# Kernel tuning notes

Measured on AMD Instinct MI355X. Metric: run time of the kernel, lower is better.

The kernel has to match this reference:

```python
import jax, jax.numpy as jnp
import numpy as np

LATENT_DIM = 64
K = 128


def setup_inputs() -> dict:
    key = jax.random.key(0)
    ks = jax.random.split(key, 7)
    B, T, N, d, k = 64, 1024, 1024, LATENT_DIM, K
    return {
        "review_seq": jax.random.normal(ks[0], (B, T, d), dtype=jnp.float32),
        "post_seq": jax.random.normal(ks[1], (B, N, d), dtype=jnp.float32),
        "Wl": jax.random.normal(ks[2], (d, d), dtype=jnp.float32) * 0.05,
        "Wr": jax.random.normal(ks[3], (k, d), dtype=jnp.float32) * 0.05,
        "Wp": jax.random.normal(ks[4], (k, d), dtype=jnp.float32) * 0.05,
        "whr": jax.random.normal(ks[5], (1, k), dtype=jnp.float32) * 0.05,
        "whp": jax.random.normal(ks[6], (1, k), dtype=jnp.float32) * 0.05,
    }


def reference(review_seq, post_seq, Wl, Wr, Wp, whr, whp):
    # L[b,t,n] = tanh(review @ Wl @ post^T)
    L = jnp.tanh(jnp.einsum('btd,dD,bnD->btn', review_seq, Wl, post_seq))
    # Hp[b,k,n] = tanh(Wp @ post^T + Wr @ review^T @ L)
    Hp = jnp.tanh(jnp.einsum('kd,bnd->bkn', Wp, post_seq)
                  + jnp.einsum('kd,btd,btn->bkn', Wr, review_seq, L))
    # Hr[b,k,t] = tanh(Wr @ review^T + Wp @ post^T @ L^T)
    Hr = jnp.tanh(jnp.einsum('kd,btd->bkt', Wr, review_seq)
                  + jnp.einsum('kd,bnd,btn->bkt', Wp, post_seq, L))
    # attention weights over post (n) and review (t) positions
    Ap = jax.nn.softmax(jnp.einsum('yk,bkn->bn', whp, Hp), axis=-1)
    Ar = jax.nn.softmax(jnp.einsum('yk,bkt->bt', whr, Hr), axis=-1)
    co_p = jnp.einsum('bnd,bn->bd', post_seq, Ap)
    co_r = jnp.einsum('btd,bt->bd', review_seq, Ar)
    return jnp.concatenate([co_p, co_r], axis=1)  # [B, 2*latent_dim]
```

## Files before the change

kernel.cpp:

```cpp
#include <hip/hip_runtime.h>
#include <hip/hip_bf16.h>


typedef __attribute__((ext_vector_type(8))) short bfrag;
typedef __attribute__((ext_vector_type(4))) float ffrag;

typedef const __attribute__((address_space(1))) unsigned GAS_U;
typedef __attribute__((address_space(3))) unsigned LAS_U;

__device__ __forceinline__ void gload16(const void* g, void* l) {
  __builtin_amdgcn_global_load_lds((GAS_U*)g, (LAS_U*)l, 16, 0, 0);
}

__device__ __forceinline__ unsigned short f2b(float f) {
  unsigned u = __builtin_bit_cast(unsigned, f);
  u += 0x7FFFu + ((u >> 16) & 1u);
  return (unsigned short)(u >> 16);
}
__device__ __forceinline__ float b2f(unsigned short h) {
  return __builtin_bit_cast(float, (unsigned)h << 16);
}
__device__ __forceinline__ float ftanh(float x) {
  float e = __builtin_amdgcn_exp2f(x * 2.88539008177792681f);
  return fmaf(-2.0f, __builtin_amdgcn_rcpf(e + 1.0f), 1.0f);
}
__device__ __forceinline__ unsigned cvtpk(float lo, float hi) {
  unsigned r;
  asm("v_cvt_pk_bf16_f32 %0, %1, %2" : "=v"(r) : "v"(lo), "v"(hi));
  return r;
}

#define MFMA(a, b, c) __builtin_amdgcn_mfma_f32_16x16x32_bf16((a), (b), (c), 0, 0, 0)


__global__ __launch_bounds__(256) void prep_kernel(
    const float* __restrict__ review, const float* __restrict__ post,
    const float* __restrict__ Wl, const float* __restrict__ Wr,
    const float* __restrict__ Wp,
    unsigned short* __restrict__ RWb, unsigned short* __restrict__ Rb,
    unsigned short* __restrict__ Pb, unsigned short* __restrict__ postb)
{
  const int chunk = blockIdx.x, b = blockIdx.y, side = blockIdx.z;
  const int tid = threadIdx.x, lane = tid & 63, w = tid >> 6;
  const int lr = lane & 15, lg = lane >> 4;
  const int r0 = chunk * 128;

  __shared__ __align__(16) unsigned short seqs[128][72];
  __shared__ __align__(16) unsigned short wgt[128][72];
  __shared__ __align__(16) unsigned short wlt[64][72];

  const float* seq = (side == 0) ? review : post;
#pragma unroll
  for (int jj = 0; jj < 8; ++jj) {
    int e = tid + jj * 256;
    int r = e >> 4, d4 = (e & 15) * 4;
    float4 v = *(const float4*)(seq + ((size_t)(b * 1024 + r0 + r)) * 64 + d4);
    unsigned lo = ((unsigned)f2b(v.y) << 16) | f2b(v.x);
    unsigned hi = ((unsigned)f2b(v.w) << 16) | f2b(v.z);
    *(uint2*)&seqs[r][d4] = make_uint2(lo, hi);
    if (side == 1)
      *(uint2*)(postb + ((size_t)(b * 1024 + r0 + r)) * 64 + d4) = make_uint2(lo, hi);
  }
  const float* wkd = (side == 0) ? Wr : Wp;
#pragma unroll
  for (int jj = 0; jj < 8; ++jj) {
    int e = tid + jj * 256;
    int k = e >> 4, d4 = (e & 15) * 4;
    float4 v = *(const float4*)(wkd + k * 64 + d4);
    unsigned lo = ((unsigned)f2b(v.y) << 16) | f2b(v.x);
    unsigned hi = ((unsigned)f2b(v.w) << 16) | f2b(v.z);
    *(uint2*)&wgt[k][d4] = make_uint2(lo, hi);
  }
  if (side == 0) {
    for (int i = tid; i < 64 * 64; i += 256) {
      int d = i >> 6, c = i & 63;
      wlt[c][d] = f2b(Wl[d * 64 + c]);
    }
  }
  __syncthreads();

  if (side == 0) {
    ffrag acc[2][4] = {};
#pragma unroll
    for (int ks = 0; ks < 2; ++ks)
#pragma unroll
      for (int is = 0; is < 4; ++is) {
        bfrag a = *(const bfrag*)&wlt[is * 16 + lr][ks * 32 + lg * 8];
#pragma unroll
        for (int tt = 0; tt < 2; ++tt) {
          bfrag bb = *(const bfrag*)&seqs[(w * 2 + tt) * 16 + lr][ks * 32 + lg * 8];
          acc[tt][is] = MFMA(a, bb, acc[tt][is]);
        }
      }
#pragma unroll
    for (int tt = 0; tt < 2; ++tt) {
      const int t = r0 + (w * 2 + tt) * 16 + lr;
      char* rowb = (char*)RWb + ((size_t)(b * 1024 + t)) * 128 + lg * 8;
#pragma unroll
      for (int is = 0; is < 4; ++is) {
        uint2 pkv;
        pkv.x = cvtpk(acc[tt][is][0], acc[tt][is][1]);
        pkv.y = cvtpk(acc[tt][is][2], acc[tt][is][3]);
        *(uint2*)(rowb + is * 32) = pkv;
      }
    }
  }
  {
    ffrag acc[2][8] = {};
#pragma unroll
    for (int ks = 0; ks < 2; ++ks)
#pragma unroll
      for (int tt = 0; tt < 2; ++tt) {
        bfrag a = *(const bfrag*)&seqs[(w * 2 + tt) * 16 + lr][ks * 32 + lg * 8];
#pragma unroll
        for (int kt = 0; kt < 8; ++kt) {
          bfrag bb = *(const bfrag*)&wgt[kt * 16 + lr][ks * 32 + lg * 8];
          acc[tt][kt] = MFMA(a, bb, acc[tt][kt]);
        }
      }
    char* dstb = (char*)((side == 0) ? Rb : Pb) + (size_t)b * 262144
                 + (size_t)(chunk * 4 + w) * 8192 + lg * 256 + lr * 16;
#pragma unroll
    for (int tt = 0; tt < 2; ++tt)
#pragma unroll
      for (int kt = 0; kt < 8; ++kt) {
        uint2 pkv;
        pkv.x = cvtpk(acc[tt][kt][0], acc[tt][kt][1]);
        pkv.y = cvtpk(acc[tt][kt][2], acc[tt][kt][3]);
        *(uint2*)(dstb + kt * 1024 + tt * 8) = pkv;
      }
  }
}

__global__ __launch_bounds__(512, 4) void hz_kernel(
    const unsigned short* __restrict__ RWb, const unsigned short* __restrict__ Rb,
    const unsigned short* __restrict__ Pb, const unsigned short* __restrict__ postb,
    const float* __restrict__ whp, const float* __restrict__ whr,
    float* __restrict__ zp, float* __restrict__ zr)
{
  const int orig = blockIdx.x;
  const int swz = (orig & 7) * 128 + (orig >> 3);
  const int strip = swz & 7, pair = swz >> 3;
  const int b = pair & 63, role = pair >> 6;
  const int s0 = strip * 128;
  const int tid = threadIdx.x, lane = tid & 63, w = tid >> 6;
  const int lr = lane & 15, lg = lane >> 4;

  const unsigned short* resident = role ? RWb : postb;
  const unsigned short* chunkseq = role ? postb : RWb;
  const unsigned short* coeff    = role ? Pb : Rb;
  const unsigned short* addterm  = role ? Rb : Pb;
  const float* wh                = role ? whr : whp;
  float* zout                    = role ? zr : zp;

  __shared__ __align__(16) char smem[24576];
  const int woff = w << 10;

  const int crow = tid >> 3, cslot = tid & 7;
  const char* csrc = (const char*)chunkseq + (size_t)b * 131072
                     + crow * 128 + ((cslot ^ (crow & 7)) << 4);
  const char* ksrc = (const char*)coeff + (size_t)b * 262144 + tid * 16;

  bfrag rb[2];
  {
    const char* rbase = (const char*)resident + ((size_t)(b * 1024 + s0)) * 128
                        + (w * 16 + lr) * 128 + lg * 16;
    rb[0] = *(const bfrag*)(rbase);
    rb[1] = *(const bfrag*)(rbase + 64);
  }

  if (w < 4) gload16(csrc, smem + woff);
  gload16(ksrc, smem + 8192 + woff);
  __syncthreads();

  ffrag acc[8] = {};

#pragma unroll 1
  for (int tc = 0; tc < 32; ++tc) {
    const int cur = tc & 1, nb = cur ^ 1;
    if (tc < 31) {
      if (w < 4) gload16(csrc + (size_t)(tc + 1) * 4096, smem + nb * 4096 + woff);
      gload16(ksrc + (size_t)(tc + 1) * 8192, smem + 8192 + nb * 8192 + woff);
    }

    const char* rwc = smem + cur * 4096;
    uint2 pk[2];
#pragma unroll
    for (int ts = 0; ts < 2; ++ts) {
      ffrag la = {};
#pragma unroll
      for (int ks = 0; ks < 2; ++ks) {
        const int arow = ts * 16 + lr;
        bfrag a = *(const bfrag*)(rwc + arow * 128 + (((ks * 4 + lg) ^ (arow & 7)) << 4));
        la = MFMA(a, rb[ks], la);
      }
      pk[ts].x = cvtpk(ftanh(la[0]), ftanh(la[1]));
      pk[ts].y = cvtpk(ftanh(la[2]), ftanh(la[3]));
    }
    uint4 au; au.x = pk[0].x; au.y = pk[0].y; au.z = pk[1].x; au.w = pk[1].y;
    const bfrag af = __builtin_bit_cast(bfrag, au);

    const char* rlc = smem + 8192 + cur * 8192 + lg * 256 + lr * 16;
#pragma unroll
    for (int kt = 0; kt < 8; ++kt) {
      bfrag bk = *(const bfrag*)(rlc + kt * 1024);
      acc[kt] = MFMA(af, bk, acc[kt]);
    }
    __syncthreads();
  }

  float whs[8];
#pragma unroll
  for (int kt = 0; kt < 8; ++kt) whs[kt] = wh[kt * 16 + lr];

  const char* abase = (const char*)addterm + (size_t)b * 262144
                      + (size_t)(strip * 4 + (w >> 1)) * 8192
                      + lg * 256 + lr * 16 + (w & 1) * 8;
  float zs[4] = {0, 0, 0, 0};
#pragma unroll
  for (int kt = 0; kt < 8; ++kt) {
    uint2 av = *(const uint2*)(abase + kt * 1024);
    const float whk = whs[kt];
    zs[0] += whk * ftanh(acc[kt][0] + b2f((unsigned short)(av.x & 0xFFFF)));
    zs[1] += whk * ftanh(acc[kt][1] + b2f((unsigned short)(av.x >> 16)));
    zs[2] += whk * ftanh(acc[kt][2] + b2f((unsigned short)(av.y & 0xFFFF)));
    zs[3] += whk * ftanh(acc[kt][3] + b2f((unsigned short)(av.y >> 16)));
  }
#pragma unroll
  for (int j = 0; j < 4; ++j) {
    zs[j] += __shfl_xor(zs[j], 1);
    zs[j] += __shfl_xor(zs[j], 2);
    zs[j] += __shfl_xor(zs[j], 4);
    zs[j] += __shfl_xor(zs[j], 8);
  }
  if (lr == 0) {
#pragma unroll
    for (int j = 0; j < 4; ++j)
      zout[(size_t)b * 1024 + s0 + w * 16 + lg * 4 + j] = zs[j];
  }
}

__global__ __launch_bounds__(1024) void final_kernel(
    const float* __restrict__ review, const float* __restrict__ post,
    const float* __restrict__ zp, const float* __restrict__ zr,
    float* __restrict__ out)
{
  const int b = blockIdx.x, side = blockIdx.y, tid = threadIdx.x;
  const int wid = tid >> 6, lane = tid & 63;
  __shared__ float zl[1024];
  __shared__ float red[16];
  __shared__ float cacc[16][64];

  const float* z = (side == 0) ? zp : zr;
  const float* seq = (side == 0) ? post : review;

  float v = z[(size_t)b * 1024 + tid];
  zl[tid] = v;
  float m = v;
#pragma unroll
  for (int off = 32; off; off >>= 1) m = fmaxf(m, __shfl_xor(m, off));
  if (lane == 0) red[wid] = m;
  __syncthreads();
  m = red[0];
#pragma unroll
  for (int i = 1; i < 16; ++i) m = fmaxf(m, red[i]);
  __syncthreads();

  float e = __expf(v - m);
  zl[tid] = e;
  float sm = e;
#pragma unroll
  for (int off = 32; off; off >>= 1) sm += __shfl_xor(sm, off);
  if (lane == 0) red[wid] = sm;
  __syncthreads();
  sm = red[0];
#pragma unroll
  for (int i = 1; i < 16; ++i) sm += red[i];
  const float inv = 1.0f / sm;

  const int d = lane;
  float a = 0.f;
  for (int n = wid * 64; n < wid * 64 + 64; ++n)
    a += zl[n] * seq[((size_t)(b * 1024 + n)) * 64 + d];
  cacc[wid][d] = a;
  __syncthreads();
  if (tid < 64) {
    float s = 0.f;
#pragma unroll
    for (int g = 0; g < 16; ++g) s += cacc[g][tid];
    out[b * 128 + side * 64 + tid] = s * inv;
  }
}

extern "C" void kernel_launch(void* const* d_in, const int* in_sizes, int n_in,
                              void* d_out, int out_size, void* d_ws, size_t ws_size,
                              hipStream_t stream) {
  const float* review = (const float*)d_in[0];
  const float* post   = (const float*)d_in[1];
  const float* Wl     = (const float*)d_in[2];
  const float* Wr     = (const float*)d_in[3];
  const float* Wp     = (const float*)d_in[4];
  const float* whr    = (const float*)d_in[5];
  const float* whp    = (const float*)d_in[6];
  float* out = (float*)d_out;

  char* ws = (char*)d_ws;
  unsigned short* RWb   = (unsigned short*)(ws);
  unsigned short* Rb    = (unsigned short*)(ws + (size_t)8  * 1048576);
  unsigned short* Pb    = (unsigned short*)(ws + (size_t)24 * 1048576);
  unsigned short* postb = (unsigned short*)(ws + (size_t)40 * 1048576);
  float* zp = (float*)(ws + (size_t)48 * 1048576);
  float* zr = (float*)(ws + (size_t)48 * 1048576 + 262144);

  prep_kernel<<<dim3(8, 64, 2), dim3(256), 0, stream>>>(
      review, post, Wl, Wr, Wp, RWb, Rb, Pb, postb);
  hz_kernel<<<dim3(1024), dim3(512), 0, stream>>>(
      RWb, Rb, Pb, postb, whp, whr, zp, zr);
  final_kernel<<<dim3(64, 2), dim3(1024), 0, stream>>>(
      review, post, zp, zr, out);
}
```

Baseline: 99.29 us.

## Double per-block strip width so each chunk load feeds two row tiles

Each hz_kernel block now covers 256 resident rows instead of 128, with each wave holding two 16-row resident fragments and two accumulator sets. Every streamed chunk of the other sequence and the coefficient matrix staged in shared memory is reused for twice as many MFMAs, which halves the global/LDS traffic for the streamed operands and halves the grid to 512 blocks. The cost is more registers per thread (two acc[8] sets) and fewer blocks to fill the GPU, which may reduce occupancy or leave CUs idle.

```diff
diff --git a/kernel.cpp b/kernel.cpp
--- a/kernel.cpp
+++ b/kernel.cpp
@@ -139,10 +139,10 @@
     float* __restrict__ zp, float* __restrict__ zr)
 {
   const int orig = blockIdx.x;
-  const int swz = (orig & 7) * 128 + (orig >> 3);
-  const int strip = swz & 7, pair = swz >> 3;
+  const int swz = (orig & 7) * 64 + (orig >> 3);
+  const int strip = swz & 3, pair = swz >> 2;
   const int b = pair & 63, role = pair >> 6;
-  const int s0 = strip * 128;
+  const int s0 = strip * 256;
   const int tid = threadIdx.x, lane = tid & 63, w = tid >> 6;
   const int lr = lane & 15, lg = lane >> 4;
 
@@ -161,19 +161,22 @@
                      + crow * 128 + ((cslot ^ (crow & 7)) << 4);
   const char* ksrc = (const char*)coeff + (size_t)b * 262144 + tid * 16;
 
-  bfrag rb[2];
+  bfrag rb[2][2];
   {
     const char* rbase = (const char*)resident + ((size_t)(b * 1024 + s0)) * 128
-                        + (w * 16 + lr) * 128 + lg * 16;
-    rb[0] = *(const bfrag*)(rbase);
-    rb[1] = *(const bfrag*)(rbase + 64);
+                        + (w * 32 + lr) * 128 + lg * 16;
+#pragma unroll
+    for (int rs = 0; rs < 2; ++rs) {
+      rb[0][rs] = *(const bfrag*)(rbase + rs * 2048);
+      rb[1][rs] = *(const bfrag*)(rbase + rs * 2048 + 64);
+    }
   }
 
   if (w < 4) gload16(csrc, smem + woff);
   gload16(ksrc, smem + 8192 + woff);
   __syncthreads();
 
-  ffrag acc[8] = {};
+  ffrag acc[2][8] = {};
 
 #pragma unroll 1
   for (int tc = 0; tc < 32; ++tc) {
@@ -184,27 +187,33 @@
     }
 
     const char* rwc = smem + cur * 4096;
-    uint2 pk[2];
+    uint2 pk[2][2];
 #pragma unroll
     for (int ts = 0; ts < 2; ++ts) {
-      ffrag la = {};
+      ffrag la0 = {}, la1 = {};
 #pragma unroll
       for (int ks = 0; ks < 2; ++ks) {
         const int arow = ts * 16 + lr;
         bfrag a = *(const bfrag*)(rwc + arow * 128 + (((ks * 4 + lg) ^ (arow & 7)) << 4));
-        la = MFMA(a, rb[ks], la);
-      }
-      pk[ts].x = cvtpk(ftanh(la[0]), ftanh(la[1]));
-      pk[ts].y = cvtpk(ftanh(la[2]), ftanh(la[3]));
-    }
-    uint4 au; au.x = pk[0].x; au.y = pk[0].y; au.z = pk[1].x; au.w = pk[1].y;
-    const bfrag af = __builtin_bit_cast(bfrag, au);
+        la0 = MFMA(a, rb[ks][0], la0);
+        la1 = MFMA(a, rb[ks][1], la1);
+      }
+      pk[ts][0].x = cvtpk(ftanh(la0[0]), ftanh(la0[1]));
+      pk[ts][0].y = cvtpk(ftanh(la0[2]), ftanh(la0[3]));
+      pk[ts][1].x = cvtpk(ftanh(la1[0]), ftanh(la1[1]));
+      pk[ts][1].y = cvtpk(ftanh(la1[2]), ftanh(la1[3]));
+    }
+    uint4 a0u; a0u.x = pk[0][0].x; a0u.y = pk[0][0].y; a0u.z = pk[1][0].x; a0u.w = pk[1][0].y;
+    uint4 a1u; a1u.x = pk[0][1].x; a1u.y = pk[0][1].y; a1u.z = pk[1][1].x; a1u.w = pk[1][1].y;
+    const bfrag af0 = __builtin_bit_cast(bfrag, a0u);
+    const bfrag af1 = __builtin_bit_cast(bfrag, a1u);
 
     const char* rlc = smem + 8192 + cur * 8192 + lg * 256 + lr * 16;
 #pragma unroll
     for (int kt = 0; kt < 8; ++kt) {
       bfrag bk = *(const bfrag*)(rlc + kt * 1024);
-      acc[kt] = MFMA(af, bk, acc[kt]);
+      acc[0][kt] = MFMA(af0, bk, acc[0][kt]);
+      acc[1][kt] = MFMA(af1, bk, acc[1][kt]);
     }
     __syncthreads();
   }
@@ -214,30 +223,32 @@
   for (int kt = 0; kt < 8; ++kt) whs[kt] = wh[kt * 16 + lr];
 
   const char* abase = (const char*)addterm + (size_t)b * 262144
-                      + (size_t)(strip * 4 + (w >> 1)) * 8192
-                      + lg * 256 + lr * 16 + (w & 1) * 8;
-  float zs[4] = {0, 0, 0, 0};
-#pragma unroll
-  for (int kt = 0; kt < 8; ++kt) {
-    uint2 av = *(const uint2*)(abase + kt * 1024);
-    const float whk = whs[kt];
-    zs[0] += whk * ftanh(acc[kt][0] + b2f((unsigned short)(av.x & 0xFFFF)));
-    zs[1] += whk * ftanh(acc[kt][1] + b2f((unsigned short)(av.x >> 16)));
-    zs[2] += whk * ftanh(acc[kt][2] + b2f((unsigned short)(av.y & 0xFFFF)));
-    zs[3] += whk * ftanh(acc[kt][3] + b2f((unsigned short)(av.y >> 16)));
-  }
-#pragma unroll
-  for (int j = 0; j < 4; ++j) {
-    zs[j] += __shfl_xor(zs[j], 1);
-    zs[j] += __shfl_xor(zs[j], 2);
-    zs[j] += __shfl_xor(zs[j], 4);
-    zs[j] += __shfl_xor(zs[j], 8);
-  }
-  if (lr == 0) {
-#pragma unroll
-    for (int j = 0; j < 4; ++j)
-      zout[(size_t)b * 1024 + s0 + w * 16 + lg * 4 + j] = zs[j];
-  }
+                      + (size_t)(strip * 8 + w) * 8192
+                      + lg * 256 + lr * 16;
+  float zs[2][4] = {};
+#pragma unroll
+  for (int rs = 0; rs < 2; ++rs)
+#pragma unroll
+    for (int kt = 0; kt < 8; ++kt) {
+      uint2 av = *(const uint2*)(abase + kt * 1024 + rs * 8);
+      const float whk = whs[kt];
+      zs[rs][0] += whk * ftanh(acc[rs][kt][0] + b2f((unsigned short)(av.x & 0xFFFF)));
+      zs[rs][1] += whk * ftanh(acc[rs][kt][1] + b2f((unsigned short)(av.x >> 16)));
+      zs[rs][2] += whk * ftanh(acc[rs][kt][2] + b2f((unsigned short)(av.y & 0xFFFF)));
+      zs[rs][3] += whk * ftanh(acc[rs][kt][3] + b2f((unsigned short)(av.y >> 16)));
+    }
+#pragma unroll
+  for (int rs = 0; rs < 2; ++rs)
+#pragma unroll
+    for (int j = 0; j < 4; ++j) {
+      float v = zs[rs][j];
+      v += __shfl_xor(v, 1);
+      v += __shfl_xor(v, 2);
+      v += __shfl_xor(v, 4);
+      v += __shfl_xor(v, 8);
+      if (lr == 0)
+        zout[(size_t)b * 1024 + s0 + w * 32 + rs * 16 + lg * 4 + j] = v;
+    }
 }
 
 __global__ __launch_bounds__(1024) void final_kernel(
@@ -314,7 +325,7 @@
 
   prep_kernel<<<dim3(8, 64, 2), dim3(256), 0, stream>>>(
       review, post, Wl, Wr, Wp, RWb, Rb, Pb, postb);
-  hz_kernel<<<dim3(1024), dim3(512), 0, stream>>>(
+  hz_kernel<<<dim3(512), dim3(512), 0, stream>>>(
       RWb, Rb, Pb, postb, whp, whr, zp, zr);
   final_kernel<<<dim3(64, 2), dim3(1024), 0, stream>>>(
       review, post, zp, zr, out);
```

New measurement: 95.19 us. -4.1%, faster.
